# Kernel optimization log

Measured on AMD Instinct MI355X. Metric: run time of the kernel, lower is better.

## Reference

```python
import jax, jax.numpy as jnp
import numpy as np

D = 6          # atom_dims, fixed by GroupNorm(2, D) and reshape(-1, 6)
K = 16         # neighbors
N_LAYERS = 3
C_IN = 2 * D + 1  # 13
EPS = 1e-5
SLOPE = 0.2


def _lrelu(x):
    return jnp.where(x >= 0, x, SLOPE * x)


def _group_norm(x, w, b):
    # x: [M, D], 2 groups of D//2 channels, affine per channel
    m = x.shape[0]
    xg = x.reshape(m, 2, D // 2)
    mu = xg.mean(-1, keepdims=True)
    var = xg.var(-1, keepdims=True)
    xn = ((xg - mu) * jax.lax.rsqrt(var + EPS)).reshape(m, D)
    return xn * w + b


def setup_inputs() -> dict:
    key = jax.random.key(0)
    ks = jax.random.split(key, 8)
    B, N = 4, 100000
    dist = jax.random.uniform(ks[0], (B, N, K, 1), dtype=jnp.float32)
    atomtypes = jax.random.uniform(ks[1], (B, N, K, D), dtype=jnp.float32)
    s1 = 1.0 / np.sqrt(C_IN)
    W1 = jax.random.uniform(ks[2], (N_LAYERS, C_IN, C_IN), jnp.float32, -s1, s1)
    b1 = jax.random.uniform(ks[3], (N_LAYERS, C_IN), jnp.float32, -s1, s1)
    W2 = jax.random.uniform(ks[4], (N_LAYERS, C_IN, D), jnp.float32, -s1, s1)
    b2 = jax.random.uniform(ks[5], (N_LAYERS, D), jnp.float32, -s1, s1)
    gw = jnp.ones((N_LAYERS, D), jnp.float32)
    gb = jnp.zeros((N_LAYERS, D), jnp.float32)
    return {"dist": dist, "atomtypes": atomtypes, "W1": W1, "b1": b1,
            "W2": W2, "b2": b2, "gw": gw, "gb": gb}


def reference(dist, atomtypes, W1, b1, W2, b2, gw, gb):
    B, N, k, d = atomtypes.shape
    point_emb = jnp.ones((B, N, d), dtype=atomtypes.dtype)
    for i in range(N_LAYERS):
        # [B,N,k,2D+1]: broadcast point emb to neighbors, concat atom feats + dist
        feat = jnp.concatenate(
            [jnp.broadcast_to(point_emb[:, :, None, :], (B, N, k, d)),
             atomtypes, dist], axis=-1)
        h = _lrelu(jnp.einsum('bnkc,cd->bnkd', feat, W1[i]) + b1[i])
        msg = (jnp.einsum('bnkc,cd->bnkd', h, W2[i]) + b2[i]).sum(-2)  # [B,N,D]
        upd = _lrelu(_group_norm(msg.reshape(-1, d), gw[i], gb[i])).reshape(B, N, d)
        point_emb = point_emb + upd
    return point_emb
```

## Files before the change

kernel.cpp:

```cpp
#include <hip/hip_runtime.h>


constexpr int DD  = 6;
constexpr int KK  = 16;
constexpr int CIN = 13;
constexpr float EPSV = 1e-5f;

__global__ __launch_bounds__(256) void atom_mp(
    const float* __restrict__ dist,
    const float* __restrict__ at,
    const float* __restrict__ W1,
    const float* __restrict__ b1,
    const float* __restrict__ W2,
    const float* __restrict__ b2,
    const float* __restrict__ gw,
    const float* __restrict__ gb,
    float* __restrict__ out,
    int P)
{
    int t = blockIdx.x * blockDim.x + threadIdx.x;
    int p = t >> 1;
    int h = t & 1;
    if (p >= P) return;

    float a[8 * DD];
    float dq[8];

    const float4* ap4 = reinterpret_cast<const float4*>(
        at + (long)p * (KK * DD) + h * (8 * DD));
    #pragma unroll
    for (int i = 0; i < 12; ++i) {
        float4 q = ap4[i];
        a[4 * i + 0] = q.x; a[4 * i + 1] = q.y;
        a[4 * i + 2] = q.z; a[4 * i + 3] = q.w;
    }
    const float4* dp4 = reinterpret_cast<const float4*>(
        dist + (long)p * KK + h * 8);
    #pragma unroll
    for (int i = 0; i < 2; ++i) {
        float4 q = dp4[i];
        dq[4 * i + 0] = q.x; dq[4 * i + 1] = q.y;
        dq[4 * i + 2] = q.z; dq[4 * i + 3] = q.w;
    }

    float pe[DD] = {1.f, 1.f, 1.f, 1.f, 1.f, 1.f};

    #pragma unroll 1
    for (int L = 0; L < 3; ++L) {
        const float* w1  = W1 + L * CIN * CIN;
        const float* w2  = W2 + L * CIN * DD;
        const float* bb1 = b1 + L * CIN;
        const float* bb2 = b2 + L * DD;
        const float* gwp = gw + L * DD;
        const float* gbp = gb + L * DD;

        float hsum[CIN];

        #pragma unroll
        for (int d = 0; d < CIN; ++d) {
            float s = bb1[d];
            #pragma unroll
            for (int c = 0; c < DD; ++c)
                s = fmaf(pe[c], w1[c * CIN + d], s);

            float w0 = w1[6 * CIN + d];
            float acc[8];
            #pragma unroll
            for (int k = 0; k < 8; ++k)
                acc[k] = fmaf(a[6 * k + 0], w0, s);
            #pragma unroll
            for (int j = 1; j < 7; ++j) {
                float w = w1[(6 + j) * CIN + d];
                #pragma unroll
                for (int k = 0; k < 8; ++k) {
                    float fv = (j < 6) ? a[6 * k + j] : dq[k];
                    acc[k] = fmaf(fv, w, acc[k]);
                }
            }
            float hs = 0.f;
            #pragma unroll
            for (int k = 0; k < 8; ++k) {
                hs = fmaf(0.6f, acc[k], hs);
                hs = fmaf(0.4f, __builtin_fabsf(acc[k]), hs);
            }
            hsum[d] = hs;
        }

        #pragma unroll
        for (int d = 0; d < CIN; ++d)
            hsum[d] += __shfl_xor(hsum[d], 1, 64);

        float msg[DD];
        #pragma unroll
        for (int d = 0; d < DD; ++d) {
            float m = 16.f * bb2[d];
            #pragma unroll
            for (int c = 0; c < CIN; ++c)
                m = fmaf(hsum[c], w2[c * DD + d], m);
            msg[d] = m;
        }

        #pragma unroll
        for (int g = 0; g < 2; ++g) {
            float m0 = msg[3 * g], m1 = msg[3 * g + 1], m2 = msg[3 * g + 2];
            float mu = (m0 + m1 + m2) * (1.f / 3.f);
            float d0 = m0 - mu, d1 = m1 - mu, d2 = m2 - mu;
            float var = (d0 * d0 + d1 * d1 + d2 * d2) * (1.f / 3.f);
            float rs = rsqrtf(var + EPSV);
            float dv[3] = {d0, d1, d2};
            #pragma unroll
            for (int c = 0; c < 3; ++c) {
                int ch = 3 * g + c;
                float xn = fmaf(dv[c] * rs, gwp[ch], gbp[ch]);
                pe[ch] = fmaf(0.6f, xn, pe[ch]);
                pe[ch] = fmaf(0.4f, __builtin_fabsf(xn), pe[ch]);
            }
        }
    }

    float* op = out + (long)p * DD;
    if (h == 0) {
        *reinterpret_cast<float2*>(op)     = make_float2(pe[0], pe[1]);
        *reinterpret_cast<float2*>(op + 2) = make_float2(pe[2], pe[3]);
    } else {
        *reinterpret_cast<float2*>(op + 4) = make_float2(pe[4], pe[5]);
    }
}

extern "C" void kernel_launch(void* const* d_in, const int* in_sizes, int n_in,
                              void* d_out, int out_size, void* d_ws, size_t ws_size,
                              hipStream_t stream) {
    const float* dist = (const float*)d_in[0];
    const float* at   = (const float*)d_in[1];
    const float* W1   = (const float*)d_in[2];
    const float* b1   = (const float*)d_in[3];
    const float* W2   = (const float*)d_in[4];
    const float* b2   = (const float*)d_in[5];
    const float* gw   = (const float*)d_in[6];
    const float* gb   = (const float*)d_in[7];
    float* out = (float*)d_out;

    int P = in_sizes[0] / KK;
    long threads_total = 2L * P;
    int threads = 256;
    int blocks = (int)((threads_total + threads - 1) / threads);
    atom_mp<<<blocks, threads, 0, stream>>>(dist, at, W1, b1, W2, b2, gw, gb, out, P);
}
```

Before: 273.6 us.

## Stage atom features in shared memory and reorder neighbor loop outermost

Result: no change. 278.0 us (+1.6%).

```diff
diff --git a/kernel.cpp b/kernel.cpp
--- a/kernel.cpp
+++ b/kernel.cpp
@@ -4,9 +4,10 @@
 constexpr int DD  = 6;
 constexpr int KK  = 16;
 constexpr int CIN = 13;
+constexpr int TPB = 256;
 constexpr float EPSV = 1e-5f;
 
-__global__ __launch_bounds__(256) void atom_mp(
+__global__ __launch_bounds__(TPB) void atom_mp(
     const float* __restrict__ dist,
     const float* __restrict__ at,
     const float* __restrict__ W1,
@@ -18,22 +19,26 @@
     float* __restrict__ out,
     int P)
 {
-    int t = blockIdx.x * blockDim.x + threadIdx.x;
-    int p = t >> 1;
-    int h = t & 1;
+    __shared__ float sa[48 * TPB];
+
+    const int tid = threadIdx.x;
+    const int t = blockIdx.x * TPB + tid;
+    const int p = t >> 1;
+    const int h = t & 1;
     if (p >= P) return;
-
-    float a[8 * DD];
-    float dq[8];
 
     const float4* ap4 = reinterpret_cast<const float4*>(
         at + (long)p * (KK * DD) + h * (8 * DD));
     #pragma unroll
     for (int i = 0; i < 12; ++i) {
         float4 q = ap4[i];
-        a[4 * i + 0] = q.x; a[4 * i + 1] = q.y;
-        a[4 * i + 2] = q.z; a[4 * i + 3] = q.w;
+        sa[(4 * i + 0) * TPB + tid] = q.x;
+        sa[(4 * i + 1) * TPB + tid] = q.y;
+        sa[(4 * i + 2) * TPB + tid] = q.z;
+        sa[(4 * i + 3) * TPB + tid] = q.w;
     }
+
+    float dq[8];
     const float4* dp4 = reinterpret_cast<const float4*>(
         dist + (long)p * KK + h * 8);
     #pragma unroll
@@ -42,6 +47,8 @@
         dq[4 * i + 0] = q.x; dq[4 * i + 1] = q.y;
         dq[4 * i + 2] = q.z; dq[4 * i + 3] = q.w;
     }
+    #pragma unroll
+    for (int i = 0; i < 8; ++i) asm volatile("" : "+v"(dq[i]));
 
     float pe[DD] = {1.f, 1.f, 1.f, 1.f, 1.f, 1.f};
 
@@ -54,38 +61,48 @@
         const float* gwp = gw + L * DD;
         const float* gbp = gb + L * DD;
 
-        float hsum[CIN];
-
+        float base[CIN];
         #pragma unroll
         for (int d = 0; d < CIN; ++d) {
             float s = bb1[d];
             #pragma unroll
             for (int c = 0; c < DD; ++c)
                 s = fmaf(pe[c], w1[c * CIN + d], s);
-
-            float w0 = w1[6 * CIN + d];
-            float acc[8];
-            #pragma unroll
-            for (int k = 0; k < 8; ++k)
-                acc[k] = fmaf(a[6 * k + 0], w0, s);
-            #pragma unroll
-            for (int j = 1; j < 7; ++j) {
-                float w = w1[(6 + j) * CIN + d];
-                #pragma unroll
-                for (int k = 0; k < 8; ++k) {
-                    float fv = (j < 6) ? a[6 * k + j] : dq[k];
-                    acc[k] = fmaf(fv, w, acc[k]);
-                }
-            }
-            float hs = 0.f;
-            #pragma unroll
-            for (int k = 0; k < 8; ++k) {
-                hs = fmaf(0.6f, acc[k], hs);
-                hs = fmaf(0.4f, __builtin_fabsf(acc[k]), hs);
-            }
-            hsum[d] = hs;
+            base[d] = s;
         }
 
+        float hs1[CIN], hs2[CIN];
+        #pragma unroll
+        for (int d = 0; d < CIN; ++d) { hs1[d] = 0.f; hs2[d] = 0.f; }
+
+        #pragma unroll
+        for (int k = 0; k < 8; ++k) {
+            const float f0 = sa[(6 * k + 0) * TPB + tid];
+            const float f1 = sa[(6 * k + 1) * TPB + tid];
+            const float f2 = sa[(6 * k + 2) * TPB + tid];
+            const float f3 = sa[(6 * k + 3) * TPB + tid];
+            const float f4 = sa[(6 * k + 4) * TPB + tid];
+            const float f5 = sa[(6 * k + 5) * TPB + tid];
+            const float fd = dq[k];
+            #pragma unroll
+            for (int d = 0; d < CIN; ++d) {
+                float x = base[d];
+                x = fmaf(f0, w1[ 6 * CIN + d], x);
+                x = fmaf(f1, w1[ 7 * CIN + d], x);
+                x = fmaf(f2, w1[ 8 * CIN + d], x);
+                x = fmaf(f3, w1[ 9 * CIN + d], x);
+                x = fmaf(f4, w1[10 * CIN + d], x);
+                x = fmaf(f5, w1[11 * CIN + d], x);
+                x = fmaf(fd, w1[12 * CIN + d], x);
+                hs1[d] += x;
+                hs2[d] += __builtin_fabsf(x);
+            }
+        }
+
+        float hsum[CIN];
+        #pragma unroll
+        for (int d = 0; d < CIN; ++d)
+            hsum[d] = fmaf(0.6f, hs1[d], 0.4f * hs2[d]);
         #pragma unroll
         for (int d = 0; d < CIN; ++d)
             hsum[d] += __shfl_xor(hsum[d], 1, 64);
@@ -142,7 +159,7 @@
 
     int P = in_sizes[0] / KK;
     long threads_total = 2L * P;
-    int threads = 256;
+    int threads = TPB;
     int blocks = (int)((threads_total + threads - 1) / threads);
     atom_mp<<<blocks, threads, 0, stream>>>(dist, at, W1, b1, W2, b2, gw, gb, out, P);
 }
```
